# Optimization experiments

Hardware: AMD Instinct MI355X
Metric: run time of the kernel (lower is better)

## Reference

```python
import jax, jax.numpy as jnp
import numpy as np
from jax import lax

# Model dims (match init_kwargs / input_specs)
E = 32      # n_routed_experts
H = 1024    # hidden_size
I = 768     # moe_intermediate_size
T = 4096    # num_tokens
K = 4       # top_k
CAP = 1024  # per-expert capacity; mean load = T*K/E = 512, std ~22 -> no overflow


def setup_inputs() -> dict:
    key = jax.random.key(0)
    k1, k2, k3, k4, k5 = jax.random.split(key, 5)
    hidden_states = jax.random.normal(k1, (T, H), jnp.float32)
    top_k_index = jax.random.randint(k2, (T, K), 0, E, dtype=jnp.int32)
    top_k_weights = jax.random.uniform(k3, (T, K), jnp.float32)
    gate_up_proj = jax.random.normal(k4, (E, 2 * I, H), jnp.float32) * 0.02
    down_proj = jax.random.normal(k5, (E, H, I), jnp.float32) * 0.02
    return {
        "hidden_states": hidden_states,
        "top_k_index": top_k_index,
        "top_k_weights": top_k_weights,
        "gate_up_proj": gate_up_proj,
        "down_proj": down_proj,
    }


def moe_forward(hidden_states, top_k_weights, gate_up_proj, down_proj, top_k_index):
    """Token-sorted grouped SwiGLU MoE, identical math to the per-expert torch loop."""
    num_tokens, hidden = hidden_states.shape
    top_k = top_k_index.shape[1]
    n_assign = num_tokens * top_k

    flat_e = top_k_index.reshape(-1)                       # [N] expert id per assignment
    flat_w = top_k_weights.reshape(-1)                     # [N]
    tok_of = jnp.arange(n_assign, dtype=jnp.int32) // top_k  # [N] source token

    # Sort assignments by expert id so each expert's tokens are contiguous.
    order = jnp.argsort(flat_e)
    s_e = flat_e[order]
    s_tok = tok_of[order]
    s_w = flat_w[order]

    counts = jnp.zeros((E,), jnp.int32).at[flat_e].add(1)          # tokens per expert
    offsets = jnp.concatenate([jnp.zeros((1,), jnp.int32),
                               jnp.cumsum(counts)[:-1].astype(jnp.int32)])

    xs = hidden_states[s_tok]                                       # [N, H] gathered inputs
    # Pad by CAP rows so fixed-size dynamic slices never clamp.
    xs_pad = jnp.concatenate([xs, jnp.zeros((CAP, hidden), xs.dtype)], axis=0)
    s_tok_pad = jnp.concatenate([s_tok, jnp.zeros((CAP,), jnp.int32)])
    s_w_pad = jnp.concatenate([s_w, jnp.zeros((CAP,), s_w.dtype)])

    def per_expert(e):
        off = offsets[e]
        chunk = lax.dynamic_slice(xs_pad, (off, 0), (CAP, hidden))   # [CAP, H]
        gu = chunk @ gate_up_proj[e].T                               # [CAP, 2I]
        gate, up = jnp.split(gu, 2, axis=-1)
        h = jax.nn.silu(gate) * up                                   # SwiGLU
        out = h @ down_proj[e].T                                     # [CAP, H]
        pos = off + jnp.arange(CAP, dtype=jnp.int32)
        valid = jnp.arange(CAP) < counts[e]
        w = jnp.where(valid, s_w_pad[pos], 0.0)
        dest = jnp.where(valid, s_tok_pad[pos], num_tokens)          # invalid -> dropped row
        return out * w[:, None], dest

    outs, dests = jax.vmap(per_expert)(jnp.arange(E))                # [E, CAP, H], [E, CAP]
    y = jnp.zeros((num_tokens + 1, hidden), hidden_states.dtype)
    y = y.at[dests.reshape(-1)].add(outs.reshape(-1, hidden))
    return y[:num_tokens]


def reference(hidden_states, top_k_index, top_k_weights, gate_up_proj, down_proj):
    return moe_forward(hidden_states, top_k_weights, gate_up_proj, down_proj, top_k_index)
```

## Files before the change

### kernel.cpp

```cpp
#include <hip/hip_runtime.h>
#include <hip/hip_bf16.h>

#define E_ 32
#define H_ 1024
#define I_ 768
#define I2_ 1536
#define T_ 4096
#define K_ 4
#define CAP_ 1024
#define NSLOT_ (E_*CAP_)

typedef __attribute__((ext_vector_type(8))) short short8;
typedef __attribute__((ext_vector_type(4))) float f32x4;

__device__ __forceinline__ short f2bf(float f) {
    __hip_bfloat16 h = __float2bfloat16(f);
    return __builtin_bit_cast(short, h);
}

typedef __attribute__((address_space(3))) void lds_void;
typedef const __attribute__((address_space(1))) void glob_void;

__device__ __forceinline__ void gload16(const void* g, void* l) {
    __builtin_amdgcn_global_load_lds((glob_void*)g, (lds_void*)l, 16, 0, 0);
}

__device__ __forceinline__ short8 cvt8(f32x4 x, f32x4 y) {
    short8 t;
    t[0]=f2bf(x[0]); t[1]=f2bf(x[1]); t[2]=f2bf(x[2]); t[3]=f2bf(x[3]);
    t[4]=f2bf(y[0]); t[5]=f2bf(y[1]); t[6]=f2bf(y[2]); t[7]=f2bf(y[3]);
    return t;
}


__global__ void k_init(int* __restrict__ cursor, int* __restrict__ s_tok,
                       float* __restrict__ s_w) {
    int i = blockIdx.x * 256 + threadIdx.x;
    if (i < E_) cursor[i] = 0;
    if (i < NSLOT_) { s_tok[i] = 0; s_w[i] = 0.f; }
}

__global__ void k_cast(const float* __restrict__ in, short* __restrict__ outb) {
    int i = blockIdx.x * 256 + threadIdx.x;
    const float* p = in + (size_t)i * 8;
    f32x4 a = *(const f32x4*)p;
    f32x4 b = *(const f32x4*)(p + 4);
    *(short8*)(outb + (size_t)i * 8) = cvt8(a, b);
}

__global__ void k_scatter(const int* __restrict__ tki, const float* __restrict__ tkw,
                          int* __restrict__ cursor, int* __restrict__ s_tok,
                          float* __restrict__ s_w, int* __restrict__ pos) {
    int n = blockIdx.x * 256 + threadIdx.x;
    if (n >= T_ * K_) return;
    int e = tki[n];
    int p = atomicAdd(cursor + e, 1);
    if (p < CAP_) {
        s_tok[e * CAP_ + p] = n >> 2;
        s_w[e * CAP_ + p]   = tkw[n];
        pos[n] = e * CAP_ + p;
    } else {
        pos[n] = -1;
    }
}

__global__ __launch_bounds__(512) void k_gemm1(
    const short* __restrict__ Xb, const float* __restrict__ W1,
    const int* __restrict__ s_tok, const int* __restrict__ counts,
    short* __restrict__ Hb)
{
    __shared__ alignas(16) short As[256 * 64];
    __shared__ alignas(16) short Bs[128 * 64];

    int bid = blockIdx.x;
    bid = (bid & 7) * (1536 / 8) + (bid >> 3);

    int e   = bid / 48;
    int rem = bid % 48;
    int mt = rem / 12, nt = rem % 12;
    int cnt = min(counts[e], CAP_);
    int row0 = mt * 256;
    if (row0 >= cnt) return;
    int gc0 = nt * 64;

    int tid = threadIdx.x, wid = tid >> 6, lane = tid & 63;
    int wm = wid >> 1, wn = wid & 1;

    unsigned offA[4];
#pragma unroll
    for (int j = 0; j < 4; ++j) {
        int cl = j * 512 + tid;
        int row = cl >> 3, cpos = cl & 7;
        int tok = s_tok[e * CAP_ + row0 + row];
        offA[j] = (unsigned)tok * H_ + ((cpos ^ (row & 7)) * 8);
    }
    const float* w1e = W1 + (size_t)e * I2_ * H_;
    unsigned gB[2]; unsigned ldsB[2];
#pragma unroll
    for (int j = 0; j < 2; ++j) {
        int cl = j * 512 + tid;
        int row = cl >> 3, cpos = cl & 7;
        int wr = (row < 64) ? (gc0 + row) : (768 + gc0 + (row - 64));
        gB[j]   = (unsigned)wr * H_ + cpos * 8;
        ldsB[j] = (unsigned)row * 64 + ((cpos ^ (row & 7)) * 8);
    }

    f32x4 accg[4][2], accu[4][2];
#pragma unroll
    for (int m = 0; m < 4; ++m)
#pragma unroll
        for (int n = 0; n < 2; ++n) {
            accg[m][n] = (f32x4){0.f, 0.f, 0.f, 0.f};
            accu[m][n] = (f32x4){0.f, 0.f, 0.f, 0.f};
        }

    for (int kt = 0; kt < H_ / 64; ++kt) {
        int k0 = kt * 64;
        f32x4 b0[2], b1[2];
#pragma unroll
        for (int j = 0; j < 2; ++j) {
            const float* p = w1e + gB[j] + k0;
            b0[j] = *(const f32x4*)p; b1[j] = *(const f32x4*)(p + 4);
        }
#pragma unroll
        for (int j = 0; j < 4; ++j)
            gload16(Xb + offA[j] + k0, (char*)As + j * 8192 + wid * 1024);
#pragma unroll
        for (int j = 0; j < 2; ++j)
            *(short8*)&Bs[ldsB[j]] = cvt8(b0[j], b1[j]);
        __syncthreads();

#pragma unroll
        for (int kk = 0; kk < 2; ++kk) {
            short8 a[4];
#pragma unroll
            for (int m = 0; m < 4; ++m) {
                int r = wm * 64 + m * 16 + (lane & 15);
                int c = (kk * 4 + (lane >> 4)) ^ (r & 7);
                a[m] = *(const short8*)&As[r * 64 + c * 8];
            }
            short8 bg[2], bu[2];
#pragma unroll
            for (int n = 0; n < 2; ++n) {
                int brg = wn * 32 + n * 16 + (lane & 15);
                int cg = (kk * 4 + (lane >> 4)) ^ (brg & 7);
                bg[n] = *(const short8*)&Bs[brg * 64 + cg * 8];
                int bru = 64 + wn * 32 + n * 16 + (lane & 15);
                int cu = (kk * 4 + (lane >> 4)) ^ (bru & 7);
                bu[n] = *(const short8*)&Bs[bru * 64 + cu * 8];
            }
#pragma unroll
            for (int m = 0; m < 4; ++m)
#pragma unroll
                for (int n = 0; n < 2; ++n) {
                    accg[m][n] = __builtin_amdgcn_mfma_f32_16x16x32_bf16(a[m], bg[n], accg[m][n], 0, 0, 0);
                    accu[m][n] = __builtin_amdgcn_mfma_f32_16x16x32_bf16(a[m], bu[n], accu[m][n], 0, 0, 0);
                }
        }
        __syncthreads();
    }

#pragma unroll
    for (int m = 0; m < 4; ++m) {
        int rb = row0 + wm * 64 + m * 16 + ((lane >> 4) * 4);
#pragma unroll
        for (int n = 0; n < 2; ++n) {
            int col = gc0 + wn * 32 + n * 16 + (lane & 15);
#pragma unroll
            for (int q = 0; q < 4; ++q) {
                float g = accg[m][n][q], u = accu[m][n][q];
                float h = (g / (1.f + __expf(-g))) * u;
                Hb[(size_t)(e * CAP_ + rb + q) * I_ + col] = f2bf(h);
            }
        }
    }
}

__global__ __launch_bounds__(512) void k_gemm2(
    const short* __restrict__ Hb, const float* __restrict__ W2,
    const float* __restrict__ s_w, const int* __restrict__ counts,
    float* __restrict__ Oslot)
{
    __shared__ alignas(16) short Ah[256 * 64];
    __shared__ alignas(16) short Bs[128 * 64];

    int bid = blockIdx.x;
    bid = (bid & 7) * (1024 / 8) + (bid >> 3);

    int e = bid / 32;
    int rem = bid % 32;
    int mt = rem / 8, nt = rem % 8;
    int cnt = min(counts[e], CAP_);
    int row0 = mt * 256;
    if (row0 >= cnt) return;
    int nc0 = nt * 128;

    int tid = threadIdx.x, wid = tid >> 6, lane = tid & 63;
    int wm = wid >> 1, wn = wid & 1;

    unsigned offA[4];
#pragma unroll
    for (int j = 0; j < 4; ++j) {
        int cl = j * 512 + tid;
        int row = cl >> 3, cpos = cl & 7;
        offA[j] = (unsigned)(e * CAP_ + row0 + row) * I_ + ((cpos ^ (row & 7)) * 8);
    }
    const float* w2e = W2 + (size_t)e * H_ * I_;
    unsigned gB[2]; unsigned ldsB[2];
#pragma unroll
    for (int j = 0; j < 2; ++j) {
        int cl = j * 512 + tid;
        int row = cl >> 3, cpos = cl & 7;
        gB[j]   = (unsigned)(nc0 + row) * I_ + cpos * 8;
        ldsB[j] = (unsigned)row * 64 + ((cpos ^ (row & 7)) * 8);
    }

    f32x4 acc[4][4];
#pragma unroll
    for (int m = 0; m < 4; ++m)
#pragma unroll
        for (int n = 0; n < 4; ++n) acc[m][n] = (f32x4){0.f, 0.f, 0.f, 0.f};

    for (int kt = 0; kt < I_ / 64; ++kt) {
        int k0 = kt * 64;
        f32x4 b0[2], b1[2];
#pragma unroll
        for (int j = 0; j < 2; ++j) {
            const float* p = w2e + gB[j] + k0;
            b0[j] = *(const f32x4*)p; b1[j] = *(const f32x4*)(p + 4);
        }
#pragma unroll
        for (int j = 0; j < 4; ++j)
            gload16(Hb + offA[j] + k0, (char*)Ah + j * 8192 + wid * 1024);
#pragma unroll
        for (int j = 0; j < 2; ++j)
            *(short8*)&Bs[ldsB[j]] = cvt8(b0[j], b1[j]);
        __syncthreads();

#pragma unroll
        for (int kk = 0; kk < 2; ++kk) {
            short8 a[4];
#pragma unroll
            for (int m = 0; m < 4; ++m) {
                int r = wm * 64 + m * 16 + (lane & 15);
                int c = (kk * 4 + (lane >> 4)) ^ (r & 7);
                a[m] = *(const short8*)&Ah[r * 64 + c * 8];
            }
            short8 b[4];
#pragma unroll
            for (int n = 0; n < 4; ++n) {
                int br = wn * 64 + n * 16 + (lane & 15);
                int c = (kk * 4 + (lane >> 4)) ^ (br & 7);
                b[n] = *(const short8*)&Bs[br * 64 + c * 8];
            }
#pragma unroll
            for (int m = 0; m < 4; ++m)
#pragma unroll
                for (int n = 0; n < 4; ++n)
                    acc[m][n] = __builtin_amdgcn_mfma_f32_16x16x32_bf16(a[m], b[n], acc[m][n], 0, 0, 0);
        }
        __syncthreads();
    }

#pragma unroll
    for (int m = 0; m < 4; ++m) {
#pragma unroll
        for (int q = 0; q < 4; ++q) {
            int i = row0 + wm * 64 + m * 16 + ((lane >> 4) * 4) + q;
            if (i < cnt) {
                float w = s_w[e * CAP_ + i];
                float* orow = Oslot + (size_t)(e * CAP_ + i) * H_;
#pragma unroll
                for (int n = 0; n < 4; ++n)
                    orow[nc0 + wn * 64 + n * 16 + (lane & 15)] = acc[m][n][q] * w;
            }
        }
    }
}

__global__ __launch_bounds__(256) void k_gather(
    const float* __restrict__ Oslot, const int* __restrict__ pos,
    float* __restrict__ out)
{
    int t = blockIdx.x;
    int c = threadIdx.x * 4;
    int p0 = pos[t * 4 + 0], p1 = pos[t * 4 + 1];
    int p2 = pos[t * 4 + 2], p3 = pos[t * 4 + 3];
    f32x4 s = (f32x4){0.f, 0.f, 0.f, 0.f};
    if (p0 >= 0) { f32x4 v = *(const f32x4*)&Oslot[(size_t)p0 * H_ + c]; s += v; }
    if (p1 >= 0) { f32x4 v = *(const f32x4*)&Oslot[(size_t)p1 * H_ + c]; s += v; }
    if (p2 >= 0) { f32x4 v = *(const f32x4*)&Oslot[(size_t)p2 * H_ + c]; s += v; }
    if (p3 >= 0) { f32x4 v = *(const f32x4*)&Oslot[(size_t)p3 * H_ + c]; s += v; }
    *(f32x4*)&out[(size_t)t * H_ + c] = s;
}


extern "C" void kernel_launch(void* const* d_in, const int* in_sizes, int n_in,
                              void* d_out, int out_size, void* d_ws, size_t ws_size,
                              hipStream_t stream) {
    const float* hs  = (const float*)d_in[0];
    const int*   tki = (const int*)d_in[1];
    const float* tkw = (const float*)d_in[2];
    const float* w1  = (const float*)d_in[3];
    const float* w2  = (const float*)d_in[4];
    float* out = (float*)d_out;

    char* ws = (char*)d_ws;
    int*   cursor = (int*)ws;
    int*   s_tok  = (int*)(ws + 4096);
    float* s_w    = (float*)(ws + 4096 + NSLOT_ * 4);
    int*   pos    = (int*)(ws + 4096 + NSLOT_ * 8);
    char*  big0   = ws + 4096 + NSLOT_ * 8 + (size_t)T_ * K_ * 4;
    short* Xb     = (short*)big0;
    short* Hb     = (short*)(big0 + (size_t)T_ * H_ * 2);
    float* Oslot  = (float*)(big0 + (size_t)T_ * H_ * 2 + (size_t)NSLOT_ * I_ * 2);

    hipLaunchKernelGGL(k_init, dim3(NSLOT_ / 256), dim3(256), 0, stream, cursor, s_tok, s_w);
    hipLaunchKernelGGL(k_cast, dim3((T_ * H_) / 2048), dim3(256), 0, stream, hs, Xb);
    hipLaunchKernelGGL(k_scatter, dim3((T_ * K_) / 256), dim3(256), 0, stream, tki, tkw, cursor, s_tok, s_w, pos);
    hipLaunchKernelGGL(k_gemm1, dim3(E_ * 4 * 12), dim3(512), 0, stream, Xb, w1, s_tok, cursor, Hb);
    hipLaunchKernelGGL(k_gemm2, dim3(E_ * 4 * 8), dim3(512), 0, stream, Hb, w2, s_w, cursor, Oslot);
    hipLaunchKernelGGL(k_gather, dim3(T_), dim3(256), 0, stream, Oslot, pos, out);
}
```

Baseline: 231.9 us.

## Load fp32 weights directly into LDS via global_load_lds and convert on read

```diff
diff --git a/kernel.cpp b/kernel.cpp
--- a/kernel.cpp
+++ b/kernel.cpp
@@ -32,20 +32,16 @@
     return t;
 }
 
-
-__global__ void k_init(int* __restrict__ cursor, int* __restrict__ s_tok,
-                       float* __restrict__ s_w) {
-    int i = blockIdx.x * 256 + threadIdx.x;
-    if (i < E_) cursor[i] = 0;
-    if (i < NSLOT_) { s_tok[i] = 0; s_w[i] = 0.f; }
-}
-
-__global__ void k_cast(const float* __restrict__ in, short* __restrict__ outb) {
-    int i = blockIdx.x * 256 + threadIdx.x;
-    const float* p = in + (size_t)i * 8;
+__global__ void k_initcast(const float* __restrict__ hs, short* __restrict__ Xb,
+                           int* __restrict__ cursor, int* __restrict__ s_tok,
+                           float* __restrict__ s_w) {
+    int g = blockIdx.x * 256 + threadIdx.x;
+    if (g < E_) cursor[g] = 0;
+    if (g < NSLOT_) { s_tok[g] = 0; s_w[g] = 0.f; }
+    const float* p = hs + (size_t)g * 8;
     f32x4 a = *(const f32x4*)p;
     f32x4 b = *(const f32x4*)(p + 4);
-    *(short8*)(outb + (size_t)i * 8) = cvt8(a, b);
+    *(short8*)(Xb + (size_t)g * 8) = cvt8(a, b);
 }
 
 __global__ void k_scatter(const int* __restrict__ tki, const float* __restrict__ tkw,
@@ -70,7 +66,7 @@
     short* __restrict__ Hb)
 {
     __shared__ alignas(16) short As[256 * 64];
-    __shared__ alignas(16) short Bs[128 * 64];
+    __shared__ alignas(16) float Bf[128 * 64];
 
     int bid = blockIdx.x;
     bid = (bid & 7) * (1536 / 8) + (bid >> 3);
@@ -95,14 +91,13 @@
         offA[j] = (unsigned)tok * H_ + ((cpos ^ (row & 7)) * 8);
     }
     const float* w1e = W1 + (size_t)e * I2_ * H_;
-    unsigned gB[2]; unsigned ldsB[2];
-#pragma unroll
-    for (int j = 0; j < 2; ++j) {
+    unsigned offB[4];
+#pragma unroll
+    for (int j = 0; j < 4; ++j) {
         int cl = j * 512 + tid;
-        int row = cl >> 3, cpos = cl & 7;
+        int row = cl >> 4, cpos = cl & 15;
         int wr = (row < 64) ? (gc0 + row) : (768 + gc0 + (row - 64));
-        gB[j]   = (unsigned)wr * H_ + cpos * 8;
-        ldsB[j] = (unsigned)row * 64 + ((cpos ^ (row & 7)) * 8);
+        offB[j] = (unsigned)wr * H_ + ((cpos ^ (row & 15)) * 4);
     }
 
     f32x4 accg[4][2], accu[4][2];
@@ -116,18 +111,12 @@
 
     for (int kt = 0; kt < H_ / 64; ++kt) {
         int k0 = kt * 64;
-        f32x4 b0[2], b1[2];
-#pragma unroll
-        for (int j = 0; j < 2; ++j) {
-            const float* p = w1e + gB[j] + k0;
-            b0[j] = *(const f32x4*)p; b1[j] = *(const f32x4*)(p + 4);
-        }
 #pragma unroll
         for (int j = 0; j < 4; ++j)
             gload16(Xb + offA[j] + k0, (char*)As + j * 8192 + wid * 1024);
 #pragma unroll
-        for (int j = 0; j < 2; ++j)
-            *(short8*)&Bs[ldsB[j]] = cvt8(b0[j], b1[j]);
+        for (int j = 0; j < 4; ++j)
+            gload16(w1e + offB[j] + k0, (char*)Bf + j * 8192 + wid * 1024);
         __syncthreads();
 
 #pragma unroll
@@ -140,14 +129,21 @@
                 a[m] = *(const short8*)&As[r * 64 + c * 8];
             }
             short8 bg[2], bu[2];
+            int i0 = (kk * 4 + (lane >> 4)) * 2;
 #pragma unroll
             for (int n = 0; n < 2; ++n) {
-                int brg = wn * 32 + n * 16 + (lane & 15);
-                int cg = (kk * 4 + (lane >> 4)) ^ (brg & 7);
-                bg[n] = *(const short8*)&Bs[brg * 64 + cg * 8];
-                int bru = 64 + wn * 32 + n * 16 + (lane & 15);
-                int cu = (kk * 4 + (lane >> 4)) ^ (bru & 7);
-                bu[n] = *(const short8*)&Bs[bru * 64 + cu * 8];
+                {
+                    int R = wn * 32 + n * 16 + (lane & 15);
+                    int p0 = i0 ^ (R & 15), p1 = (i0 + 1) ^ (R & 15);
+                    bg[n] = cvt8(*(const f32x4*)&Bf[R * 64 + p0 * 4],
+                                 *(const f32x4*)&Bf[R * 64 + p1 * 4]);
+                }
+                {
+                    int R = 64 + wn * 32 + n * 16 + (lane & 15);
+                    int p0 = i0 ^ (R & 15), p1 = (i0 + 1) ^ (R & 15);
+                    bu[n] = cvt8(*(const f32x4*)&Bf[R * 64 + p0 * 4],
+                                 *(const f32x4*)&Bf[R * 64 + p1 * 4]);
+                }
             }
 #pragma unroll
             for (int m = 0; m < 4; ++m)
@@ -182,7 +178,7 @@
     float* __restrict__ Oslot)
 {
     __shared__ alignas(16) short Ah[256 * 64];
-    __shared__ alignas(16) short Bs[128 * 64];
+    __shared__ alignas(16) float Bf[128 * 64];
 
     int bid = blockIdx.x;
     bid = (bid & 7) * (1024 / 8) + (bid >> 3);
@@ -206,13 +202,12 @@
         offA[j] = (unsigned)(e * CAP_ + row0 + row) * I_ + ((cpos ^ (row & 7)) * 8);
     }
     const float* w2e = W2 + (size_t)e * H_ * I_;
-    unsigned gB[2]; unsigned ldsB[2];
-#pragma unroll
-    for (int j = 0; j < 2; ++j) {
+    unsigned offB[4];
+#pragma unroll
+    for (int j = 0; j < 4; ++j) {
         int cl = j * 512 + tid;
-        int row = cl >> 3, cpos = cl & 7;
-        gB[j]   = (unsigned)(nc0 + row) * I_ + cpos * 8;
-        ldsB[j] = (unsigned)row * 64 + ((cpos ^ (row & 7)) * 8);
+        int row = cl >> 4, cpos = cl & 15;
+        offB[j] = (unsigned)(nc0 + row) * I_ + ((cpos ^ (row & 15)) * 4);
     }
 
     f32x4 acc[4][4];
@@ -223,18 +218,12 @@
 
     for (int kt = 0; kt < I_ / 64; ++kt) {
         int k0 = kt * 64;
-        f32x4 b0[2], b1[2];
-#pragma unroll
-        for (int j = 0; j < 2; ++j) {
-            const float* p = w2e + gB[j] + k0;
-            b0[j] = *(const f32x4*)p; b1[j] = *(const f32x4*)(p + 4);
-        }
 #pragma unroll
         for (int j = 0; j < 4; ++j)
             gload16(Hb + offA[j] + k0, (char*)Ah + j * 8192 + wid * 1024);
 #pragma unroll
-        for (int j = 0; j < 2; ++j)
-            *(short8*)&Bs[ldsB[j]] = cvt8(b0[j], b1[j]);
+        for (int j = 0; j < 4; ++j)
+            gload16(w2e + offB[j] + k0, (char*)Bf + j * 8192 + wid * 1024);
         __syncthreads();
 
 #pragma unroll
@@ -247,11 +236,13 @@
                 a[m] = *(const short8*)&Ah[r * 64 + c * 8];
             }
             short8 b[4];
+            int i0 = (kk * 4 + (lane >> 4)) * 2;
 #pragma unroll
             for (int n = 0; n < 4; ++n) {
-                int br = wn * 64 + n * 16 + (lane & 15);
-                int c = (kk * 4 + (lane >> 4)) ^ (br & 7);
-                b[n] = *(const short8*)&Bs[br * 64 + c * 8];
+                int R = wn * 64 + n * 16 + (lane & 15);
+                int p0 = i0 ^ (R & 15), p1 = (i0 + 1) ^ (R & 15);
+                b[n] = cvt8(*(const f32x4*)&Bf[R * 64 + p0 * 4],
+                            *(const f32x4*)&Bf[R * 64 + p1 * 4]);
             }
 #pragma unroll
             for (int m = 0; m < 4; ++m)
@@ -287,10 +278,10 @@
     int p0 = pos[t * 4 + 0], p1 = pos[t * 4 + 1];
     int p2 = pos[t * 4 + 2], p3 = pos[t * 4 + 3];
     f32x4 s = (f32x4){0.f, 0.f, 0.f, 0.f};
-    if (p0 >= 0) { f32x4 v = *(const f32x4*)&Oslot[(size_t)p0 * H_ + c]; s += v; }
-    if (p1 >= 0) { f32x4 v = *(const f32x4*)&Oslot[(size_t)p1 * H_ + c]; s += v; }
-    if (p2 >= 0) { f32x4 v = *(const f32x4*)&Oslot[(size_t)p2 * H_ + c]; s += v; }
-    if (p3 >= 0) { f32x4 v = *(const f32x4*)&Oslot[(size_t)p3 * H_ + c]; s += v; }
+    if (p0 >= 0) s += *(const f32x4*)&Oslot[(size_t)p0 * H_ + c];
+    if (p1 >= 0) s += *(const f32x4*)&Oslot[(size_t)p1 * H_ + c];
+    if (p2 >= 0) s += *(const f32x4*)&Oslot[(size_t)p2 * H_ + c];
+    if (p3 >= 0) s += *(const f32x4*)&Oslot[(size_t)p3 * H_ + c];
     *(f32x4*)&out[(size_t)t * H_ + c] = s;
 }
 
@@ -315,9 +306,10 @@
     short* Hb     = (short*)(big0 + (size_t)T_ * H_ * 2);
     float* Oslot  = (float*)(big0 + (size_t)T_ * H_ * 2 + (size_t)NSLOT_ * I_ * 2);
 
-    hipLaunchKernelGGL(k_init, dim3(NSLOT_ / 256), dim3(256), 0, stream, cursor, s_tok, s_w);
-    hipLaunchKernelGGL(k_cast, dim3((T_ * H_) / 2048), dim3(256), 0, stream, hs, Xb);
-    hipLaunchKernelGGL(k_scatter, dim3((T_ * K_) / 256), dim3(256), 0, stream, tki, tkw, cursor, s_tok, s_w, pos);
+    hipLaunchKernelGGL(k_initcast, dim3((T_ * H_) / 2048), dim3(256), 0, stream,
+                       hs, Xb, cursor, s_tok, s_w);
+    hipLaunchKernelGGL(k_scatter, dim3((T_ * K_) / 256), dim3(256), 0, stream,
+                       tki, tkw, cursor, s_tok, s_w, pos);
     hipLaunchKernelGGL(k_gemm1, dim3(E_ * 4 * 12), dim3(512), 0, stream, Xb, w1, s_tok, cursor, Hb);
     hipLaunchKernelGGL(k_gemm2, dim3(E_ * 4 * 8), dim3(512), 0, stream, Hb, w2, s_w, cursor, Oslot);
     hipLaunchKernelGGL(k_gather, dim3(T_), dim3(256), 0, stream, Oslot, pos, out);
```

Result: slower. 303.2 us (+30.7%).
